# Kernel optimization log

Hardware: AMD Instinct MI355X
Metric: run time of the kernel (lower is better)

Reference implementation:

```python
import jax, jax.numpy as jnp
import numpy as np

BETA = 0.25


def setup_inputs() -> dict:
    key = jax.random.key(0)
    k1, k2 = jax.random.split(key)
    z = jax.random.normal(k1, (16, 64, 32, 32), dtype=jnp.float32)
    emb_w = jax.random.normal(k2, (16384, 64), dtype=jnp.float32)
    return {"z": z, "emb_w": emb_w}


def reference(z, emb_w):
    # z: [b, c, h, w] with c == embed_dim; emb_w: [n_embed, embed_dim]
    b, c, h, w = z.shape
    zc = jnp.transpose(z, (0, 2, 3, 1))          # [b, h, w, c]
    zf = zc.reshape(-1, c)                        # [N, c]
    # squared euclidean distances: ||z||^2 - 2 z E^T + ||E||^2  -> [N, n_embed]
    d = (jnp.sum(zf * zf, axis=1, keepdims=True)
         - 2.0 * (zf @ emb_w.T)
         + jnp.sum(emb_w * emb_w, axis=1))
    idx = jnp.argmin(d, axis=1)                   # [N]
    z_q = emb_w[idx].reshape(zc.shape)            # [b, h, w, c]
    # commitment loss (codebook side detached, eval-mode forward)
    loss = BETA * jnp.mean((jax.lax.stop_gradient(z_q) - zc) ** 2)
    # straight-through estimator
    z_q_ste = zc + jax.lax.stop_gradient(z_q - zc)
    z_q_out = jnp.transpose(z_q_ste, (0, 3, 1, 2))  # back to bchw
    return (z_q_out, loss)
```

## Files before the change

kernel.cpp:

```cpp
#include <hip/hip_runtime.h>
#include <math.h>

#define NQ      16384
#define NE      16384
#define DIM     64
#define QB      128
#define CS1     8
#define CPB1    (NE / CS1)
#define CPW1    (CPB1 / 4)
#define NT1     (CPW1 / 16)
#define THREADS 256
#define EPS     0.4f

typedef _Float16 half8 __attribute__((ext_vector_type(8)));
typedef float    f32x4 __attribute__((ext_vector_type(4)));
typedef unsigned int       uint32;
typedef unsigned short     uint16;
typedef unsigned long long uint64;

#define W_NORMS   0
#define W_PM1     16384
#define W_PM2     147456
#define W_PG      278528
#define W_FINALG  344064
#define W_RLIST   360448
#define W_COUNT   376832
#define W_LOSSP   376848
#define W_RKEY    377104
#define W_ZH1     409872
#define W_ZH2     934160
#define W_EH1     1458448
#define W_EH2     1982736

__device__ inline uint32 fmono(float f) {
    uint32 u = __float_as_uint(f);
    return (u & 0x80000000u) ? ~u : (u | 0x80000000u);
}

__global__ __launch_bounds__(THREADS)
void vq_prep(const float* __restrict__ z, const float* __restrict__ emb,
             _Float16* __restrict__ zh1, _Float16* __restrict__ zh2,
             _Float16* __restrict__ eh1, _Float16* __restrict__ eh2,
             float* __restrict__ norms, uint32* __restrict__ count) {
    if (blockIdx.x == 0 && threadIdx.x == 0) *count = 0u;
    if (blockIdx.x < 64) {
        int e = blockIdx.x * THREADS + threadIdx.x;
        const float4* row = reinterpret_cast<const float4*>(emb + (size_t)e * DIM);
        float s = 0.f;
#pragma unroll
        for (int i = 0; i < DIM / 4; ++i) {
            float4 v = row[i];
            s = fmaf(v.x, v.x, s); s = fmaf(v.y, v.y, s);
            s = fmaf(v.z, v.z, s); s = fmaf(v.w, v.w, s);
            union { _Float16 h[4]; uint2 u; } p1, p2;
            float f[4] = {-2.f * v.x, -2.f * v.y, -2.f * v.z, -2.f * v.w};
#pragma unroll
            for (int j = 0; j < 4; ++j) {
                _Float16 h1 = (_Float16)f[j];
                p1.h[j] = h1;
                p2.h[j] = (_Float16)(f[j] - (float)h1);
            }
            *reinterpret_cast<uint2*>(eh1 + (size_t)e * DIM + i * 4) = p1.u;
            *reinterpret_cast<uint2*>(eh2 + (size_t)e * DIM + i * 4) = p2.u;
        }
        norms[e] = s;
    } else {
        int n = (blockIdx.x - 64) * THREADS + threadIdx.x;
        const float* zp = z + (size_t)(n >> 10) * 65536 + (n & 1023);
#pragma unroll 8
        for (int c = 0; c < DIM; ++c) {
            float x = zp[(size_t)c * 1024];
            _Float16 h1 = (_Float16)x;
            _Float16 h2 = (_Float16)(x - (float)h1);
            zh1[(size_t)n * DIM + c] = h1;
            zh2[(size_t)n * DIM + c] = h2;
        }
    }
}

#define LOADA(S, TL) {                                                            \
    const _Float16* _p = eh1 + (size_t)(cwbase + (TL) * 16 + r15) * DIM + hk * 8; \
    A##S##0 = *reinterpret_cast<const half8*>(_p);                                \
    A##S##1 = *reinterpret_cast<const half8*>(_p + 32);                           \
    N##S = *reinterpret_cast<const f32x4*>(norms + cwbase + (TL) * 16 + hk * 4); }

#define COMPUTE(S, TL) {                                                          \
    f32x4 acc[8];                                                                 \
    __builtin_amdgcn_s_setprio(1);                                                \
    _Pragma("unroll")                                                             \
    for (int qt = 0; qt < 8; ++qt) {                                              \
        acc[qt] = __builtin_amdgcn_mfma_f32_16x16x32_f16(A##S##0, B1[qt][0], N##S,    0, 0, 0); \
        acc[qt] = __builtin_amdgcn_mfma_f32_16x16x32_f16(A##S##1, B1[qt][1], acc[qt], 0, 0, 0); \
    }                                                                             \
    __builtin_amdgcn_s_setprio(0);                                                \
    const uint32 _tid = (uint32)(TL);                                             \
    _Pragma("unroll")                                                             \
    for (int qt = 0; qt < 8; ++qt) {                                              \
        float v = fminf(fminf(fminf(acc[qt][0], acc[qt][1]), acc[qt][2]), acc[qt][3]); \
        float nm2 = fminf(m2[qt], fmaxf(v, mv[qt]));             \
        bool lt = v < mv[qt];                            \
        mv[qt] = lt ? v : mv[qt];                                                 \
        mi[qt] = lt ? _tid : mi[qt];                                              \
        m2[qt] = nm2;                                                             \
    } }

__global__ __launch_bounds__(THREADS, 2)
void vq_pass1(const _Float16* __restrict__ zh1, const _Float16* __restrict__ eh1,
              const float* __restrict__ norms,
              float* __restrict__ pm1, float* __restrict__ pm2, uint16* __restrict__ pg) {
    __shared__ float  redv[4][QB];
    __shared__ float  red2[4][QB];
    __shared__ uint32 redg[4][QB];

    const int t    = threadIdx.x;
    const int lane = t & 63;
    const int wave = t >> 6;
    const int r15  = lane & 15, hk = lane >> 4;
    const int qbase  = blockIdx.x * QB;
    const int cwbase = blockIdx.y * CPB1 + wave * CPW1;

    half8 B1[8][2];
#pragma unroll
    for (int qt = 0; qt < 8; ++qt)
#pragma unroll
        for (int kc = 0; kc < 2; ++kc)
            B1[qt][kc] = *reinterpret_cast<const half8*>(
                zh1 + (size_t)(qbase + qt * 16 + r15) * DIM + kc * 32 + hk * 8);

    float  mv[8], m2[8];
    uint32 mi[8];
#pragma unroll
    for (int q = 0; q < 8; ++q) { mv[q] = INFINITY; m2[q] = INFINITY; mi[q] = 0u; }

    half8 A00, A01, A10, A11, A20, A21, A30, A31;
    f32x4 N0, N1, N2, N3;

    LOADA(0, 0)
    LOADA(1, 1)
    for (int tb = 0; tb < NT1; tb += 4) {
        LOADA(2, tb + 2)
        LOADA(3, tb + 3)
        COMPUTE(0, tb)
        COMPUTE(1, tb + 1)
        int t4 = (tb + 4 < NT1) ? tb + 4 : 0;
        int t5 = (tb + 5 < NT1) ? tb + 5 : 0;
        LOADA(0, t4)
        LOADA(1, t5)
        COMPUTE(2, tb + 2)
        COMPUTE(3, tb + 3)
    }

    uint32 gi[8];
#pragma unroll
    for (int q = 0; q < 8; ++q)
        gi[q] = (uint32)(cwbase >> 2) + (mi[q] << 2) + (uint32)hk;

#pragma unroll
    for (int st = 16; st < 64; st <<= 1) {
#pragma unroll
        for (int q = 0; q < 8; ++q) {
            float  ov  = __shfl_xor(mv[q], st, 64);
            float  o2  = __shfl_xor(m2[q], st, 64);
            uint32 og  = (uint32)__shfl_xor((int)gi[q], st, 64);
            float nm2 = fminf(fminf(m2[q], o2), fmaxf(mv[q], ov));
            if (ov < mv[q] || (ov == mv[q] && og < gi[q])) { mv[q] = ov; gi[q] = og; }
            m2[q] = nm2;
        }
    }
    if (lane < 16) {
#pragma unroll
        for (int qt = 0; qt < 8; ++qt) {
            redv[wave][qt * 16 + lane] = mv[qt];
            red2[wave][qt * 16 + lane] = m2[qt];
            redg[wave][qt * 16 + lane] = gi[qt];
        }
    }
    __syncthreads();

    if (t < QB) {
        float  bv = redv[0][t], b2 = red2[0][t];
        uint32 bg = redg[0][t];
#pragma unroll
        for (int w = 1; w < 4; ++w) {
            float v = redv[w][t], s2 = red2[w][t];
            float nm2 = fminf(fminf(b2, s2), fmaxf(bv, v));
            if (v < bv) { bv = v; bg = redg[w][t]; }
            b2 = nm2;
        }
        pm1[(size_t)blockIdx.y * NQ + qbase + t] = bv;
        pm2[(size_t)blockIdx.y * NQ + qbase + t] = b2;
        pg [(size_t)blockIdx.y * NQ + qbase + t] = (uint16)bg;
    }
}

__global__ __launch_bounds__(THREADS)
void vq_select(const float* __restrict__ pm1, const float* __restrict__ pm2,
               const uint16* __restrict__ pg,
               uint32* __restrict__ final_g, uint32* __restrict__ rlist,
               uint32* __restrict__ count, uint64* __restrict__ rkey) {
    const int n = blockIdx.x * THREADS + threadIdx.x;
    float M1 = INFINITY, M2 = INFINITY;
    uint32 G = 0u;
#pragma unroll
    for (int s = 0; s < CS1; ++s) {
        float  m1  = pm1[(size_t)s * NQ + n];
        float  m2s = pm2[(size_t)s * NQ + n];
        uint32 g   = (uint32)pg[(size_t)s * NQ + n];
        float nm2 = fminf(fminf(M2, m2s), fmaxf(M1, m1));
        if (m1 < M1) { M1 = m1; G = g; }
        M2 = nm2;
    }
    rkey[n] = ~0ull;
    if (M2 - M1 > EPS) {
        final_g[n] = G;
    } else {
        final_g[n] = 0xFFFFFFFFu;
        uint32 p = atomicAdd(count, 1u);
        rlist[p] = (uint32)n;
    }
}

__global__ __launch_bounds__(THREADS, 2)
void vq_rescue(const _Float16* __restrict__ zh1, const _Float16* __restrict__ zh2,
               const _Float16* __restrict__ eh1, const _Float16* __restrict__ eh2,
               const float* __restrict__ norms,
               const uint32* __restrict__ rlist, const uint32* __restrict__ countp,
               uint64* __restrict__ rkey) {
    __shared__ float  redv[4][QB];
    __shared__ uint32 redg[4][QB];

    const uint32 count = *countp;
    const uint32 nch   = (count + 127u) >> 7;
    const int t    = threadIdx.x;
    const int lane = t & 63;
    const int wave = t >> 6;
    const int r15  = lane & 15, hk = lane >> 4;
    const int cy   = blockIdx.x & 15;
    const int rcb  = cy * 1024 + wave * 256;

    for (uint32 cx = (uint32)(blockIdx.x >> 4); cx < nch; cx += 32u) {
        half8 B1[8][2], B2[8][2];
#pragma unroll
        for (int qt = 0; qt < 8; ++qt) {
            uint32 j = cx * 128u + (uint32)(qt * 16 + r15);
            uint32 qid = (j < count) ? rlist[j] : 0u;
#pragma unroll
            for (int kc = 0; kc < 2; ++kc) {
                size_t off = (size_t)qid * DIM + kc * 32 + hk * 8;
                B1[qt][kc] = *reinterpret_cast<const half8*>(zh1 + off);
                B2[qt][kc] = *reinterpret_cast<const half8*>(zh2 + off);
            }
        }

        float  mv[8];
        uint32 mi[8];
#pragma unroll
        for (int q = 0; q < 8; ++q) { mv[q] = INFINITY; mi[q] = 0u; }

        half8 a1[2], a2[2];
        f32x4 nc;
        {
            const _Float16* p1 = eh1 + (size_t)(rcb + r15) * DIM + hk * 8;
            const _Float16* p2 = eh2 + (size_t)(rcb + r15) * DIM + hk * 8;
            a1[0] = *reinterpret_cast<const half8*>(p1);
            a1[1] = *reinterpret_cast<const half8*>(p1 + 32);
            a2[0] = *reinterpret_cast<const half8*>(p2);
            a2[1] = *reinterpret_cast<const half8*>(p2 + 32);
            nc = *reinterpret_cast<const f32x4*>(norms + rcb + hk * 4);
        }

#pragma unroll 2
        for (int tile = 0; tile < 16; ++tile) {
            int nt = (tile + 1 < 16) ? tile + 1 : tile;
            half8 b1[2], b2[2];
            f32x4 nn;
            {
                const _Float16* p1 = eh1 + (size_t)(rcb + nt * 16 + r15) * DIM + hk * 8;
                const _Float16* p2 = eh2 + (size_t)(rcb + nt * 16 + r15) * DIM + hk * 8;
                b1[0] = *reinterpret_cast<const half8*>(p1);
                b1[1] = *reinterpret_cast<const half8*>(p1 + 32);
                b2[0] = *reinterpret_cast<const half8*>(p2);
                b2[1] = *reinterpret_cast<const half8*>(p2 + 32);
                nn = *reinterpret_cast<const f32x4*>(norms + rcb + nt * 16 + hk * 4);
            }

            f32x4 acc[8];
            __builtin_amdgcn_s_setprio(1);
#pragma unroll
            for (int qt = 0; qt < 8; ++qt) {
                acc[qt] = __builtin_amdgcn_mfma_f32_16x16x32_f16(a1[0], B1[qt][0], nc,      0, 0, 0);
                acc[qt] = __builtin_amdgcn_mfma_f32_16x16x32_f16(a1[1], B1[qt][1], acc[qt], 0, 0, 0);
                acc[qt] = __builtin_amdgcn_mfma_f32_16x16x32_f16(a1[0], B2[qt][0], acc[qt], 0, 0, 0);
                acc[qt] = __builtin_amdgcn_mfma_f32_16x16x32_f16(a1[1], B2[qt][1], acc[qt], 0, 0, 0);
                acc[qt] = __builtin_amdgcn_mfma_f32_16x16x32_f16(a2[0], B1[qt][0], acc[qt], 0, 0, 0);
                acc[qt] = __builtin_amdgcn_mfma_f32_16x16x32_f16(a2[1], B1[qt][1], acc[qt], 0, 0, 0);
            }
            __builtin_amdgcn_s_setprio(0);

            const uint32 tid = (uint32)tile;
#pragma unroll
            for (int qt = 0; qt < 8; ++qt) {
                float v = fminf(fminf(fminf(acc[qt][0], acc[qt][1]), acc[qt][2]), acc[qt][3]);
                bool lt = v < mv[qt];
                mv[qt] = lt ? v : mv[qt];
                mi[qt] = lt ? tid : mi[qt];
            }
            a1[0] = b1[0]; a1[1] = b1[1];
            a2[0] = b2[0]; a2[1] = b2[1];
            nc = nn;
        }

        uint32 gi[8];
#pragma unroll
        for (int q = 0; q < 8; ++q)
            gi[q] = (uint32)(rcb >> 2) + (mi[q] << 2) + (uint32)hk;
#pragma unroll
        for (int st = 16; st < 64; st <<= 1) {
#pragma unroll
            for (int q = 0; q < 8; ++q) {
                float  ov = __shfl_xor(mv[q], st, 64);
                uint32 og = (uint32)__shfl_xor((int)gi[q], st, 64);
                if (ov < mv[q] || (ov == mv[q] && og < gi[q])) { mv[q] = ov; gi[q] = og; }
            }
        }
        if (lane < 16) {
#pragma unroll
            for (int qt = 0; qt < 8; ++qt) {
                redv[wave][qt * 16 + lane] = mv[qt];
                redg[wave][qt * 16 + lane] = gi[qt];
            }
        }
        __syncthreads();
        if (t < QB) {
            float  bv = redv[0][t];
            uint32 bg = redg[0][t];
#pragma unroll
            for (int w = 1; w < 4; ++w) {
                float v = redv[w][t];
                if (v < bv) { bv = v; bg = redg[w][t]; }
            }
            uint32 j = cx * 128u + (uint32)t;
            if (j < count) {
                uint64 key = ((uint64)fmono(bv) << 32) | (uint64)bg;
                atomicMin(rkey + rlist[j], key);
            }
        }
        __syncthreads();
    }
}

__global__ __launch_bounds__(THREADS)
void vq_finalize(const float* __restrict__ z,
                 const float* __restrict__ emb,
                 const float* __restrict__ norms,
                 const uint32* __restrict__ final_g,
                 const uint64* __restrict__ rkey,
                 float* __restrict__ out,
                 float* __restrict__ lossp) {
    const int t  = threadIdx.x;
    const int ql = t >> 2, p = t & 3;
    const int n  = blockIdx.x * 64 + ql;
    const int c0 = p * 16;

    uint32 bg = final_g[n];
    if (bg == 0xFFFFFFFFu) bg = (uint32)(rkey[n] & 0xFFFFFFFFull);

    const float* zp = z + (size_t)(n >> 10) * 65536 + (n & 1023);
    float zq[16];
#pragma unroll
    for (int c = 0; c < 16; ++c) zq[c] = zp[(size_t)(c0 + c) * 1024];

    float dp[4];
#pragma unroll
    for (int j = 0; j < 4; ++j) {
        const float4* er = reinterpret_cast<const float4*>(emb + (size_t)(bg * 4 + j) * DIM + c0);
        float d = 0.f;
#pragma unroll
        for (int i = 0; i < 4; ++i) {
            float4 e4 = er[i];
            d = fmaf(e4.x, zq[i * 4 + 0], d);
            d = fmaf(e4.y, zq[i * 4 + 1], d);
            d = fmaf(e4.z, zq[i * 4 + 2], d);
            d = fmaf(e4.w, zq[i * 4 + 3], d);
        }
        dp[j] = d;
    }
#pragma unroll
    for (int st = 1; st < 4; st <<= 1) {
#pragma unroll
        for (int j = 0; j < 4; ++j) dp[j] += __shfl_xor(dp[j], st, 64);
    }

    float4 nr = *reinterpret_cast<const float4*>(norms + bg * 4);
    float nra[4] = {nr.x, nr.y, nr.z, nr.w};
    float bs = INFINITY;
    uint32 bi = 0u;
#pragma unroll
    for (int j = 0; j < 4; ++j) {
        float s = fmaf(-2.f, dp[j], nra[j]);
        if (s < bs) { bs = s; bi = bg * 4 + j; }
    }

    const float* ew = emb + (size_t)bi * DIM + c0;
    float* op = out + (size_t)(n >> 10) * 65536 + (n & 1023);

    float ls = 0.f;
#pragma unroll
    for (int c = 0; c < 16; ++c) {
        float e = ew[c];
        op[(size_t)(c0 + c) * 1024] = e;
        float d = e - zq[c];
        ls = fmaf(d, d, ls);
    }

#pragma unroll
    for (int off = 32; off > 0; off >>= 1) ls += __shfl_down(ls, off, 64);
    __shared__ float wsum[THREADS / 64];
    if ((t & 63) == 0) wsum[t >> 6] = ls;
    __syncthreads();
    if (t == 0) {
        float s = 0.f;
#pragma unroll
        for (int w = 0; w < THREADS / 64; ++w) s += wsum[w];
        lossp[blockIdx.x] = s;
    }
}

__global__ __launch_bounds__(64)
void vq_loss_final(const float* __restrict__ lossp, float* __restrict__ out) {
    float v = 0.f;
#pragma unroll
    for (int k = 0; k < 4; ++k) v += lossp[threadIdx.x + k * 64];
#pragma unroll
    for (int off = 32; off > 0; off >>= 1) v += __shfl_down(v, off, 64);
    if (threadIdx.x == 0)
        out[1048576] = 0.25f * v / 1048576.0f;
}

extern "C" void kernel_launch(void* const* d_in, const int* in_sizes, int n_in,
                              void* d_out, int out_size, void* d_ws, size_t ws_size,
                              hipStream_t stream) {
    const float* z   = (const float*)d_in[0];
    const float* emb = (const float*)d_in[1];
    float* out = (float*)d_out;

    float* ws = (float*)d_ws;
    float*     norms   = ws + W_NORMS;
    float*     pm1     = ws + W_PM1;
    float*     pm2     = ws + W_PM2;
    uint16*    pg      = (uint16*)(ws + W_PG);
    uint32*    final_g = (uint32*)(ws + W_FINALG);
    uint32*    rlist   = (uint32*)(ws + W_RLIST);
    uint32*    count   = (uint32*)(ws + W_COUNT);
    float*     lossp   = ws + W_LOSSP;
    uint64*    rkey    = (uint64*)(ws + W_RKEY);
    _Float16*  zh1     = (_Float16*)(ws + W_ZH1);
    _Float16*  zh2     = (_Float16*)(ws + W_ZH2);
    _Float16*  eh1     = (_Float16*)(ws + W_EH1);
    _Float16*  eh2     = (_Float16*)(ws + W_EH2);

    vq_prep<<<128, THREADS, 0, stream>>>(z, emb, zh1, zh2, eh1, eh2, norms, count);

    dim3 g1(NQ / QB, CS1);
    vq_pass1<<<g1, THREADS, 0, stream>>>(zh1, eh1, norms, pm1, pm2, pg);

    vq_select<<<NQ / THREADS, THREADS, 0, stream>>>(pm1, pm2, pg, final_g, rlist, count, rkey);

    vq_rescue<<<512, THREADS, 0, stream>>>(zh1, zh2, eh1, eh2, norms, rlist, count, rkey);

    vq_finalize<<<NQ / 64, THREADS, 0, stream>>>(z, emb, norms, final_g, rkey, out, lossp);
    vq_loss_final<<<1, 64, 0, stream>>>(lossp, out);
}
```

Baseline: 97.03 us.

## Switch pass-1 distance GEMM to 32x32x16 MFMA with 16-code groups

Pass 1 moves from 16x16x32 MFMA tiles to 32x32x16 tiles. Each lane now takes the min over 16 accumulator values, which covers a group of 16 codes, and the codebook is split into 4 chunks instead of 8. This cuts the number of partial-min entries and the cross-lane shuffle reduction work. The finalize kernel has to rescore 16 candidate codes per group instead of 4, which adds dot-product work in that stage. The workspace offsets are shrunk to match the smaller partial arrays.

```diff
diff --git a/kernel.cpp b/kernel.cpp
--- a/kernel.cpp
+++ b/kernel.cpp
@@ -5,32 +5,35 @@
 #define NE      16384
 #define DIM     64
 #define QB      128
-#define CS1     8
+#define CS1     4
 #define CPB1    (NE / CS1)
 #define CPW1    (CPB1 / 4)
-#define NT1     (CPW1 / 16)
+#define NT1     (CPW1 / 32)
 #define THREADS 256
 #define EPS     0.4f
 
-typedef _Float16 half8 __attribute__((ext_vector_type(8)));
-typedef float    f32x4 __attribute__((ext_vector_type(4)));
+typedef _Float16 half8  __attribute__((ext_vector_type(8)));
+typedef float    f32x4  __attribute__((ext_vector_type(4)));
+typedef float    f32x16 __attribute__((ext_vector_type(16)));
 typedef unsigned int       uint32;
 typedef unsigned short     uint16;
 typedef unsigned long long uint64;
 
+typedef union { f32x16 v; f32x4 q[4]; } nvec16;
+
 #define W_NORMS   0
 #define W_PM1     16384
-#define W_PM2     147456
-#define W_PG      278528
-#define W_FINALG  344064
-#define W_RLIST   360448
-#define W_COUNT   376832
-#define W_LOSSP   376848
-#define W_RKEY    377104
-#define W_ZH1     409872
-#define W_ZH2     934160
-#define W_EH1     1458448
-#define W_EH2     1982736
+#define W_PM2     81920
+#define W_PG      147456
+#define W_FINALG  180224
+#define W_RLIST   196608
+#define W_COUNT   212992
+#define W_LOSSP   213008
+#define W_RKEY    213264
+#define W_ZH1     246032
+#define W_ZH2     770320
+#define W_EH1     1294608
+#define W_EH2     1818896
 
 __device__ inline uint32 fmono(float f) {
     uint32 u = __float_as_uint(f);
@@ -78,30 +81,40 @@
     }
 }
 
-#define LOADA(S, TL) {                                                            \
-    const _Float16* _p = eh1 + (size_t)(cwbase + (TL) * 16 + r15) * DIM + hk * 8; \
-    A##S##0 = *reinterpret_cast<const half8*>(_p);                                \
-    A##S##1 = *reinterpret_cast<const half8*>(_p + 32);                           \
-    N##S = *reinterpret_cast<const f32x4*>(norms + cwbase + (TL) * 16 + hk * 4); }
-
-#define COMPUTE(S, TL) {                                                          \
-    f32x4 acc[8];                                                                 \
-    __builtin_amdgcn_s_setprio(1);                                                \
-    _Pragma("unroll")                                                             \
-    for (int qt = 0; qt < 8; ++qt) {                                              \
-        acc[qt] = __builtin_amdgcn_mfma_f32_16x16x32_f16(A##S##0, B1[qt][0], N##S,    0, 0, 0); \
-        acc[qt] = __builtin_amdgcn_mfma_f32_16x16x32_f16(A##S##1, B1[qt][1], acc[qt], 0, 0, 0); \
-    }                                                                             \
-    __builtin_amdgcn_s_setprio(0);                                                \
-    const uint32 _tid = (uint32)(TL);                                             \
-    _Pragma("unroll")                                                             \
-    for (int qt = 0; qt < 8; ++qt) {                                              \
-        float v = fminf(fminf(fminf(acc[qt][0], acc[qt][1]), acc[qt][2]), acc[qt][3]); \
-        float nm2 = fminf(m2[qt], fmaxf(v, mv[qt]));             \
-        bool lt = v < mv[qt];                            \
-        mv[qt] = lt ? v : mv[qt];                                                 \
-        mi[qt] = lt ? _tid : mi[qt];                                              \
-        m2[qt] = nm2;                                                             \
+#define LOADT(AS, NS, TL) {                                                        \
+    const _Float16* _pa = eh1 + (size_t)(cwbase + (TL) * 32 + q31) * DIM + hi8;    \
+    AS[0] = *reinterpret_cast<const half8*>(_pa);                                  \
+    AS[1] = *reinterpret_cast<const half8*>(_pa + 16);                             \
+    AS[2] = *reinterpret_cast<const half8*>(_pa + 32);                             \
+    AS[3] = *reinterpret_cast<const half8*>(_pa + 48);                             \
+    const float* _pn = norms + cwbase + (TL) * 32 + hi4;                           \
+    NS.q[0] = *reinterpret_cast<const f32x4*>(_pn);                                \
+    NS.q[1] = *reinterpret_cast<const f32x4*>(_pn + 8);                            \
+    NS.q[2] = *reinterpret_cast<const f32x4*>(_pn + 16);                           \
+    NS.q[3] = *reinterpret_cast<const f32x4*>(_pn + 24); }
+
+#define COMPUTE(AS, NS, TL) {                                                      \
+    const uint32 _tid = (uint32)(TL);                                              \
+    _Pragma("unroll")                                                              \
+    for (int qg = 0; qg < 4; ++qg) {                                               \
+        f32x16 acc;                                                                \
+        __builtin_amdgcn_s_setprio(1);                                             \
+        acc = __builtin_amdgcn_mfma_f32_32x32x16_f16(AS[0], B[qg][0], NS.v, 0, 0, 0); \
+        acc = __builtin_amdgcn_mfma_f32_32x32x16_f16(AS[1], B[qg][1], acc,  0, 0, 0); \
+        acc = __builtin_amdgcn_mfma_f32_32x32x16_f16(AS[2], B[qg][2], acc,  0, 0, 0); \
+        acc = __builtin_amdgcn_mfma_f32_32x32x16_f16(AS[3], B[qg][3], acc,  0, 0, 0); \
+        __builtin_amdgcn_s_setprio(0);                                             \
+        float u0 = fminf(fminf(acc[0],  acc[1]),  acc[2]);                         \
+        float u1 = fminf(fminf(acc[3],  acc[4]),  acc[5]);                         \
+        float u2 = fminf(fminf(acc[6],  acc[7]),  acc[8]);                         \
+        float u3 = fminf(fminf(acc[9],  acc[10]), acc[11]);                        \
+        float u4 = fminf(fminf(acc[12], acc[13]), acc[14]);                        \
+        float v  = fminf(fminf(fminf(u0, u1), u2), fminf(fminf(u3, u4), acc[15])); \
+        float nm2 = fminf(m2[qg], fmaxf(v, mv[qg]));              \
+        bool lt = v < mv[qg];                             \
+        mv[qg] = lt ? v : mv[qg];                                                  \
+        mi[qg] = lt ? _tid : mi[qg];                                               \
+        m2[qg] = nm2;                                                              \
     } }
 
 __global__ __launch_bounds__(THREADS, 2)
@@ -115,64 +128,57 @@
     const int t    = threadIdx.x;
     const int lane = t & 63;
     const int wave = t >> 6;
-    const int r15  = lane & 15, hk = lane >> 4;
+    const int q31  = lane & 31;
+    const int hi   = lane >> 5;
+    const int hi8  = hi * 8;
+    const int hi4  = hi * 4;
     const int qbase  = blockIdx.x * QB;
     const int cwbase = blockIdx.y * CPB1 + wave * CPW1;
 
-    half8 B1[8][2];
-#pragma unroll
-    for (int qt = 0; qt < 8; ++qt)
-#pragma unroll
-        for (int kc = 0; kc < 2; ++kc)
-            B1[qt][kc] = *reinterpret_cast<const half8*>(
-                zh1 + (size_t)(qbase + qt * 16 + r15) * DIM + kc * 32 + hk * 8);
-
-    float  mv[8], m2[8];
-    uint32 mi[8];
-#pragma unroll
-    for (int q = 0; q < 8; ++q) { mv[q] = INFINITY; m2[q] = INFINITY; mi[q] = 0u; }
-
-    half8 A00, A01, A10, A11, A20, A21, A30, A31;
-    f32x4 N0, N1, N2, N3;
-
-    LOADA(0, 0)
-    LOADA(1, 1)
-    for (int tb = 0; tb < NT1; tb += 4) {
-        LOADA(2, tb + 2)
-        LOADA(3, tb + 3)
-        COMPUTE(0, tb)
-        COMPUTE(1, tb + 1)
-        int t4 = (tb + 4 < NT1) ? tb + 4 : 0;
-        int t5 = (tb + 5 < NT1) ? tb + 5 : 0;
-        LOADA(0, t4)
-        LOADA(1, t5)
-        COMPUTE(2, tb + 2)
-        COMPUTE(3, tb + 3)
-    }
-
-    uint32 gi[8];
-#pragma unroll
-    for (int q = 0; q < 8; ++q)
-        gi[q] = (uint32)(cwbase >> 2) + (mi[q] << 2) + (uint32)hk;
-
-#pragma unroll
-    for (int st = 16; st < 64; st <<= 1) {
-#pragma unroll
-        for (int q = 0; q < 8; ++q) {
-            float  ov  = __shfl_xor(mv[q], st, 64);
-            float  o2  = __shfl_xor(m2[q], st, 64);
-            uint32 og  = (uint32)__shfl_xor((int)gi[q], st, 64);
-            float nm2 = fminf(fminf(m2[q], o2), fmaxf(mv[q], ov));
-            if (ov < mv[q] || (ov == mv[q] && og < gi[q])) { mv[q] = ov; gi[q] = og; }
-            m2[q] = nm2;
-        }
-    }
-    if (lane < 16) {
-#pragma unroll
-        for (int qt = 0; qt < 8; ++qt) {
-            redv[wave][qt * 16 + lane] = mv[qt];
-            red2[wave][qt * 16 + lane] = m2[qt];
-            redg[wave][qt * 16 + lane] = gi[qt];
+    half8 B[4][4];
+#pragma unroll
+    for (int qg = 0; qg < 4; ++qg)
+#pragma unroll
+        for (int kc = 0; kc < 4; ++kc)
+            B[qg][kc] = *reinterpret_cast<const half8*>(
+                zh1 + (size_t)(qbase + qg * 32 + q31) * DIM + kc * 16 + hi8);
+
+    float  mv[4], m2[4];
+    uint32 mi[4];
+#pragma unroll
+    for (int q = 0; q < 4; ++q) { mv[q] = INFINITY; m2[q] = INFINITY; mi[q] = 0u; }
+
+    half8  A0[4], A1[4];
+    nvec16 N0, N1;
+
+    LOADT(A0, N0, 0)
+    for (int tb = 0; tb < NT1; tb += 2) {
+        LOADT(A1, N1, tb + 1)
+        COMPUTE(A0, N0, tb)
+        LOADT(A0, N0, (tb + 2 < NT1) ? tb + 2 : 0)
+        COMPUTE(A1, N1, tb + 1)
+    }
+
+    uint32 gi[4];
+#pragma unroll
+    for (int qg = 0; qg < 4; ++qg)
+        gi[qg] = ((uint32)(cwbase >> 5) + mi[qg]) * 2u + (uint32)hi;
+
+#pragma unroll
+    for (int qg = 0; qg < 4; ++qg) {
+        float  ov = __shfl_xor(mv[qg], 32, 64);
+        float  o2 = __shfl_xor(m2[qg], 32, 64);
+        uint32 og = (uint32)__shfl_xor((int)gi[qg], 32, 64);
+        float nm2 = fminf(fminf(m2[qg], o2), fmaxf(mv[qg], ov));
+        if (ov < mv[qg] || (ov == mv[qg] && og < gi[qg])) { mv[qg] = ov; gi[qg] = og; }
+        m2[qg] = nm2;
+    }
+    if (lane < 32) {
+#pragma unroll
+        for (int qg = 0; qg < 4; ++qg) {
+            redv[wave][qg * 32 + lane] = mv[qg];
+            red2[wave][qg * 32 + lane] = m2[qg];
+            redg[wave][qg * 32 + lane] = gi[qg];
         }
     }
     __syncthreads();
@@ -363,17 +369,22 @@
     const int c0 = p * 16;
 
     uint32 bg = final_g[n];
-    if (bg == 0xFFFFFFFFu) bg = (uint32)(rkey[n] & 0xFFFFFFFFull);
+    if (bg == 0xFFFFFFFFu) {
+        uint32 c4 = (uint32)(rkey[n] & 0xFFFFFFFFull) * 4u;
+        bg = (c4 >> 5) * 2u + ((c4 >> 2) & 1u);
+    }
+    const int gbase = (int)((bg >> 1) * 32u + (bg & 1u) * 4u);
 
     const float* zp = z + (size_t)(n >> 10) * 65536 + (n & 1023);
     float zq[16];
 #pragma unroll
     for (int c = 0; c < 16; ++c) zq[c] = zp[(size_t)(c0 + c) * 1024];
 
-    float dp[4];
-#pragma unroll
-    for (int j = 0; j < 4; ++j) {
-        const float4* er = reinterpret_cast<const float4*>(emb + (size_t)(bg * 4 + j) * DIM + c0);
+    float dp[16];
+#pragma unroll
+    for (int j = 0; j < 16; ++j) {
+        int code = gbase + (j & 3) + 8 * (j >> 2);
+        const float4* er = reinterpret_cast<const float4*>(emb + (size_t)code * DIM + c0);
         float d = 0.f;
 #pragma unroll
         for (int i = 0; i < 4; ++i) {
@@ -388,17 +399,21 @@
 #pragma unroll
     for (int st = 1; st < 4; st <<= 1) {
 #pragma unroll
-        for (int j = 0; j < 4; ++j) dp[j] += __shfl_xor(dp[j], st, 64);
-    }
-
-    float4 nr = *reinterpret_cast<const float4*>(norms + bg * 4);
-    float nra[4] = {nr.x, nr.y, nr.z, nr.w};
+        for (int j = 0; j < 16; ++j) dp[j] += __shfl_xor(dp[j], st, 64);
+    }
+
+    f32x4 nr[4];
+#pragma unroll
+    for (int k = 0; k < 4; ++k)
+        nr[k] = *reinterpret_cast<const f32x4*>(norms + gbase + k * 8);
+
     float bs = INFINITY;
     uint32 bi = 0u;
 #pragma unroll
-    for (int j = 0; j < 4; ++j) {
-        float s = fmaf(-2.f, dp[j], nra[j]);
-        if (s < bs) { bs = s; bi = bg * 4 + j; }
+    for (int j = 0; j < 16; ++j) {
+        float s = fmaf(-2.f, dp[j], nr[j >> 2][j & 3]);
+        uint32 code = (uint32)(gbase + (j & 3) + 8 * (j >> 2));
+        if (s < bs) { bs = s; bi = code; }
     }
 
     const float* ew = emb + (size_t)bi * DIM + c0;
```

New measurement: 94.50 us. 2.6% less time.
